# Optimization experiments

Hardware: AMD Instinct MI355X
Metric: run time of the kernel (lower is better)

## Reference

```python
import jax, jax.numpy as jnp
import numpy as np

SOFTMAX_TEMP = 0.01  # config['networks']['matcher_block']['softmax_temp']
B, WINDOW, C, N, WIDTH = 2, 2, 64, 400, 256


def setup_inputs() -> dict:
    key = jax.random.key(0)
    k1, k2, k3 = jax.random.split(key, 3)
    BW = B * WINDOW
    keypoint_scores = jax.random.uniform(k1, (BW, 1, N), dtype=jnp.float32)
    keypoint_desc = jax.random.normal(k2, (BW, C, N), dtype=jnp.float32)
    desc_dense = jax.random.normal(k3, (BW, C, WIDTH, WIDTH), dtype=jnp.float32)
    # pairing indices exactly as built in SoftmaxRefMatcher.__init__
    tgt_ids, src_ids = [], []
    for b in range(B):
        for w in range(WINDOW - 1):
            for t in range(w + 1, WINDOW):
                src_ids.append(w + b * WINDOW)
                tgt_ids.append(t + b * WINDOW)
    return {
        "keypoint_scores": keypoint_scores,
        "keypoint_desc": keypoint_desc,
        "desc_dense": desc_dense,
        "tgt_ids": jnp.array(tgt_ids, dtype=jnp.int32),
        "src_ids": jnp.array(src_ids, dtype=jnp.int32),
    }


def _l2_normalize(x):
    # F.normalize(x, dim=1), eps=1e-12
    return x / jnp.maximum(jnp.linalg.norm(x, axis=1, keepdims=True), 1e-12)


def reference(keypoint_scores, keypoint_desc, desc_dense, tgt_ids, src_ids):
    BW, Cdim, H, W = desc_dense.shape
    HW = H * W
    # src_coords_dense: meshgrid('ij') -> coords[k] = (u=k%W, v=k//W)
    hw = jnp.arange(HW)
    coords = jnp.stack([(hw % W).astype(jnp.float32),
                        (hw // W).astype(jnp.float32)], axis=1)  # [HW, 2]

    src_desc = _l2_normalize(desc_dense.reshape(BW, Cdim, HW))[src_ids]  # [P, C, HW]
    tgt_desc = _l2_normalize(keypoint_desc)[tgt_ids]                     # [P, C, N]

    match_vals = jnp.einsum('pcn,pcm->pnm', tgt_desc, src_desc)          # [P, N, HW]
    soft_match = jax.nn.softmax(match_vals / SOFTMAX_TEMP, axis=2)
    pseudo_coords = jnp.einsum('pnm,mk->pnk', soft_match, coords)        # [P, N, 2]

    tgt_scores = keypoint_scores[tgt_ids]
    return pseudo_coords, tgt_scores, tgt_ids, src_ids
```

## Files before the change

kernel.cpp:

```cpp
#include <hip/hip_runtime.h>
#include <math.h>

#define NPAIR  2
#define KDIM   64
#define NKP    400
#define NPADR  448
#define DSTR   14
#define HWPIX  65536
#define MREF   70.0f
#define LOG2E  1.44269504f

#define AFRAG_DW (NPAIR*DSTR*2*2*2*256)

using frag_ab = __attribute__((ext_vector_type(8))) short;
using f32x4   = __attribute__((ext_vector_type(4))) float;

__device__ __forceinline__ unsigned short f2bf(float f){
    unsigned u = __builtin_bit_cast(unsigned, f);
    u += 0x7fffu + ((u >> 16) & 1u);
    return (unsigned short)(u >> 16);
}
__device__ __forceinline__ float bf2f(unsigned short h){
    unsigned u = ((unsigned)h) << 16;
    return __builtin_bit_cast(float, u);
}
__device__ __forceinline__ float red16(float v){
    v += __builtin_bit_cast(float, __builtin_amdgcn_update_dpp(0, __builtin_bit_cast(int, v), 0xB1,  0xF, 0xF, true));
    v += __builtin_bit_cast(float, __builtin_amdgcn_update_dpp(0, __builtin_bit_cast(int, v), 0x4E,  0xF, 0xF, true));
    v += __builtin_bit_cast(float, __builtin_amdgcn_update_dpp(0, __builtin_bit_cast(int, v), 0x141, 0xF, 0xF, true));
    v += __builtin_bit_cast(float, __builtin_amdgcn_update_dpp(0, __builtin_bit_cast(int, v), 0x140, 0xF, 0xF, true));
    return v;
}

__global__ __launch_bounds__(256) void prep_kernel(
    const float* __restrict__ ksc, const float* __restrict__ kd,
    const int* __restrict__ tgt_ids, const int* __restrict__ src_ids,
    unsigned* __restrict__ wsu, float* __restrict__ out)
{
    __shared__ float xs[KDIM][33];
    __shared__ float inv_s[32];
    int d = blockIdx.x, p = blockIdx.y, t = threadIdx.x;
    int tgt = tgt_ids[p];
    int nl = t & 31, c0 = t >> 5;
    #pragma unroll
    for (int cc = 0; cc < 8; ++cc){
        int c = cc*8 + c0;
        int n = d*32 + nl;
        xs[c][nl] = (n < NKP) ? kd[(tgt*KDIM + c)*NKP + n] : 0.f;
    }
    __syncthreads();
    if (t < 32){
        float s = 0.f;
        #pragma unroll
        for (int c = 0; c < KDIM; ++c){ float v = xs[c][t]; s = fmaf(v, v, s); }
        inv_s[t] = 1.f / fmaxf(sqrtf(s), 1e-12f);
    }
    __syncthreads();
    {
        int l = t & 63, rk = t >> 6;
        int rt = rk >> 1, ks = rk & 1;
        int cl = l & 15, g = l >> 4;
        int nloc = rt*16 + cl;
        float inv = inv_s[nloc];
        int k0 = ks*32 + g*8;
        unsigned hu[4], lu[4];
        #pragma unroll
        for (int j2 = 0; j2 < 4; ++j2){
            float xa = xs[k0 + 2*j2    ][nloc] * inv;
            float xb = xs[k0 + 2*j2 + 1][nloc] * inv;
            unsigned short ha = f2bf(xa), hb = f2bf(xb);
            unsigned short la = f2bf(xa - bf2f(ha)), lb = f2bf(xb - bf2f(hb));
            hu[j2] = (unsigned)ha | ((unsigned)hb << 16);
            lu[j2] = (unsigned)la | ((unsigned)lb << 16);
        }
        unsigned base = (unsigned)((((p*DSTR + d)*2 + rt)*2 + ks)*2)*256 + l*4;
        *(uint4*)&wsu[base]       = make_uint4(hu[0], hu[1], hu[2], hu[3]);
        *(uint4*)&wsu[base + 256] = make_uint4(lu[0], lu[1], lu[2], lu[3]);
    }
    if (t < 32){
        int n = d*32 + t;
        if (n < NKP) out[NPAIR*NKP*2 + p*NKP + n] = ksc[tgt*NKP + n];
    }
    if (d == 0 && t == 0){
        out[NPAIR*NKP*3 + p]         = (float)tgt;
        out[NPAIR*NKP*3 + NPAIR + p] = (float)src_ids[p];
    }
}

__global__ __launch_bounds__(256, 4) void match_kernel(
    const float* __restrict__ dd, const int* __restrict__ src_ids,
    const unsigned* __restrict__ wsu, float* __restrict__ part)
{
    __shared__ unsigned lds[8192];
    __shared__ float ssp[256];
    __shared__ float invn_s[128];
    int mb = blockIdx.x, p = blockIdx.y, t = threadIdx.x;
    const float* plane = dd + (size_t)src_ids[p]*KDIM*HWPIX + mb*128;

    {
        int m = t & 127, kh = t >> 7;
        unsigned sw7 = (unsigned)(m & 7) << 2;
        float ssum = 0.f;
        #pragma unroll
        for (int s2l = 0; s2l < 4; ++s2l){
            int s2 = kh*4 + s2l;
            float v[8];
            #pragma unroll
            for (int j = 0; j < 8; ++j) v[j] = plane[(size_t)(s2*8 + j)*HWPIX + m];
            unsigned hq[4], lq[4];
            #pragma unroll
            for (int q = 0; q < 4; ++q){
                float a = v[2*q], b = v[2*q + 1];
                ssum = fmaf(a, a, ssum);
                ssum = fmaf(b, b, ssum);
                unsigned short ha = f2bf(a), hb = f2bf(b);
                unsigned short la = f2bf(a - bf2f(ha)), lb = f2bf(b - bf2f(hb));
                hq[q] = (unsigned)ha | ((unsigned)hb << 16);
                lq[q] = (unsigned)la | ((unsigned)lb << 16);
            }
            unsigned dwb = (unsigned)m*32 + (((unsigned)s2 << 2) ^ sw7);
            *(uint4*)&lds[dwb]        = make_uint4(hq[0], hq[1], hq[2], hq[3]);
            *(uint4*)&lds[4096 + dwb] = make_uint4(lq[0], lq[1], lq[2], lq[3]);
        }
        ssp[t] = ssum;
    }
    __syncthreads();
    if (t < 128)
        invn_s[t] = (100.f * LOG2E) / fmaxf(sqrtf(ssp[t] + ssp[t + 128]), 1e-12f);
    __syncthreads();

    int w = t >> 6, l = t & 63;
    int cl = l & 15, g = l >> 4;
    int mq = w & 1;
    int mtb = mq << 2;
    const float mref2 = MREF * LOG2E;
    float invm[4];
    #pragma unroll
    for (int mi = 0; mi < 4; ++mi) invm[mi] = invn_s[(mtb + mi)*16 + cl];

    #pragma unroll 1
    for (int d = (w >> 1); d < DSTR; d += 2){
        uint4 AH[2][2], AL[2][2];
        #pragma unroll
        for (int rt = 0; rt < 2; ++rt)
        #pragma unroll
        for (int ks = 0; ks < 2; ++ks){
            unsigned base = (unsigned)((((p*DSTR + d)*2 + rt)*2 + ks)*2)*256 + l*4;
            AH[rt][ks] = *(const uint4*)&wsu[base];
            AL[rt][ks] = *(const uint4*)&wsu[base + 256];
        }
        f32x4 acc[2][4];
        #pragma unroll
        for (int rt = 0; rt < 2; ++rt)
            #pragma unroll
            for (int mi = 0; mi < 4; ++mi)
                acc[rt][mi] = (f32x4){0.f, 0.f, 0.f, 0.f};

        #pragma unroll
        for (int ks = 0; ks < 2; ++ks){
            frag_ab aH0 = __builtin_bit_cast(frag_ab, AH[0][ks]);
            frag_ab aL0 = __builtin_bit_cast(frag_ab, AL[0][ks]);
            frag_ab aH1 = __builtin_bit_cast(frag_ab, AH[1][ks]);
            frag_ab aL1 = __builtin_bit_cast(frag_ab, AL[1][ks]);
            #pragma unroll
            for (int mi = 0; mi < 4; ++mi){
                int mrow = (mtb + mi)*16 + cl;
                unsigned swm = (unsigned)(mrow & 7) << 2;
                unsigned dwb = (unsigned)mrow*32 + (((unsigned)(ks*4 + g) << 2) ^ swm);
                frag_ab BH = __builtin_bit_cast(frag_ab, *(const uint4*)&lds[dwb]);
                frag_ab BL = __builtin_bit_cast(frag_ab, *(const uint4*)&lds[4096 + dwb]);
                acc[0][mi] = __builtin_amdgcn_mfma_f32_16x16x32_bf16(aH0, BH, acc[0][mi], 0, 0, 0);
                acc[1][mi] = __builtin_amdgcn_mfma_f32_16x16x32_bf16(aH1, BH, acc[1][mi], 0, 0, 0);
                acc[0][mi] = __builtin_amdgcn_mfma_f32_16x16x32_bf16(aH0, BL, acc[0][mi], 0, 0, 0);
                acc[1][mi] = __builtin_amdgcn_mfma_f32_16x16x32_bf16(aH1, BL, acc[1][mi], 0, 0, 0);
                acc[0][mi] = __builtin_amdgcn_mfma_f32_16x16x32_bf16(aL0, BH, acc[0][mi], 0, 0, 0);
                acc[1][mi] = __builtin_amdgcn_mfma_f32_16x16x32_bf16(aL1, BH, acc[1][mi], 0, 0, 0);
            }
        }
        #pragma unroll
        for (int rt = 0; rt < 2; ++rt)
        #pragma unroll
        for (int r = 0; r < 4; ++r){
            float sE = 0.f, sU = 0.f;
            #pragma unroll
            for (int mi = 0; mi < 4; ++mi){
                float e = exp2f(fmaf(acc[rt][mi][r], invm[mi], -mref2));
                sE += e;
                sU = fmaf(e, (float)(mi*16), sU);
            }
            sU = fmaf((float)cl, sE, sU);
            sE = red16(sE); sU = red16(sU);
            if (cl == 0){
                int n = d*32 + rt*16 + g*4 + r;
                *(float2*)&part[(((size_t)(p*NPADR + n)*512 + mb)*2 + mq)*2] =
                    make_float2(sE, sU);
            }
        }
    }
}

__global__ __launch_bounds__(256) void merge_kernel(
    const float* __restrict__ part, float* __restrict__ out)
{
    int wid = blockIdx.x*4 + (threadIdx.x >> 6);
    int l = threadIdx.x & 63;
    int p = wid / NKP, n = wid - p*NKP;
    const float* base = part + (size_t)(p*NPADR + n)*2048;
    float S = 0.f, U = 0.f, V = 0.f;
    #pragma unroll
    for (int k = 0; k < 8; ++k){
        int mbk = l + 64*k;
        float4 q = *(const float4*)&base[mbk*4];
        float u0 = (float)((mbk & 1)*128);
        float s = q.x + q.z;
        S += s;
        U += q.y + q.w + u0*q.x + (u0 + 64.f)*q.z;
        V = fmaf((float)(mbk >> 1), s, V);
    }
    #pragma unroll
    for (int off = 1; off < 64; off <<= 1){
        S += __shfl_xor(S, off);
        U += __shfl_xor(U, off);
        V += __shfl_xor(V, off);
    }
    if (l == 0){
        out[(p*NKP + n)*2 + 0] = U / S;
        out[(p*NKP + n)*2 + 1] = V / S;
    }
}

extern "C" void kernel_launch(void* const* d_in, const int* in_sizes, int n_in,
                              void* d_out, int out_size, void* d_ws, size_t ws_size,
                              hipStream_t stream)
{
    const float* ksc     = (const float*)d_in[0];
    const float* kd      = (const float*)d_in[1];
    const float* dd      = (const float*)d_in[2];
    const int*   tgt_ids = (const int*)d_in[3];
    const int*   src_ids = (const int*)d_in[4];
    float* out = (float*)d_out;
    unsigned* wsu = (unsigned*)d_ws;
    float* part = (float*)d_ws + AFRAG_DW;

    prep_kernel <<<dim3(DSTR, NPAIR), 256, 0, stream>>>(ksc, kd, tgt_ids, src_ids, wsu, out);
    match_kernel<<<dim3(512,  NPAIR), 256, 0, stream>>>(dd, src_ids, wsu, part);
    merge_kernel<<<200,               256, 0, stream>>>(part, out);
}
```

Before: 138.3 us.

## Software-pipeline match kernel: hoist B fragments, prefetch A, overlap MFMA with epilogue

```diff
diff --git a/kernel.cpp b/kernel.cpp
--- a/kernel.cpp
+++ b/kernel.cpp
@@ -87,7 +87,7 @@
     }
 }
 
-__global__ __launch_bounds__(256, 4) void match_kernel(
+__global__ __launch_bounds__(256, 3) void match_kernel(
     const float* __restrict__ dd, const int* __restrict__ src_ids,
     const unsigned* __restrict__ wsu, float* __restrict__ part)
 {
@@ -95,6 +95,19 @@
     __shared__ float ssp[256];
     __shared__ float invn_s[128];
     int mb = blockIdx.x, p = blockIdx.y, t = threadIdx.x;
+    int w = t >> 6, l = t & 63;
+    int cl = l & 15, g = l >> 4;
+    int mq = w & 1;
+    int rt = (w >> 1) & 1;
+    int mtb = mq << 2;
+
+    const unsigned* wA = wsu + (size_t)p*28672 + rt*1024 + (unsigned)l*4;
+    uint4 Ae[4], Ao[4];
+    #pragma unroll
+    for (int k = 0; k < 4; ++k) Ae[k] = *(const uint4*)(wA + 0*2048 + k*256);
+    #pragma unroll
+    for (int k = 0; k < 4; ++k) Ao[k] = *(const uint4*)(wA + 1*2048 + k*256);
+
     const float* plane = dd + (size_t)src_ids[p]*KDIM*HWPIX + mb*128;
 
     {
@@ -129,74 +142,80 @@
         invn_s[t] = (100.f * LOG2E) / fmaxf(sqrtf(ssp[t] + ssp[t + 128]), 1e-12f);
     __syncthreads();
 
-    int w = t >> 6, l = t & 63;
-    int cl = l & 15, g = l >> 4;
-    int mq = w & 1;
-    int mtb = mq << 2;
     const float mref2 = MREF * LOG2E;
     float invm[4];
     #pragma unroll
     for (int mi = 0; mi < 4; ++mi) invm[mi] = invn_s[(mtb + mi)*16 + cl];
 
-    #pragma unroll 1
-    for (int d = (w >> 1); d < DSTR; d += 2){
-        uint4 AH[2][2], AL[2][2];
-        #pragma unroll
-        for (int rt = 0; rt < 2; ++rt)
+    uint4 Bf[2][4][2];
+    #pragma unroll
+    for (int ks = 0; ks < 2; ++ks)
+    #pragma unroll
+    for (int mi = 0; mi < 4; ++mi){
+        int mrow = (mtb + mi)*16 + cl;
+        unsigned swm = (unsigned)(mrow & 7) << 2;
+        unsigned dwb = (unsigned)mrow*32 + (((unsigned)(ks*4 + g) << 2) ^ swm);
+        Bf[ks][mi][0] = *(const uint4*)&lds[dwb];
+        Bf[ks][mi][1] = *(const uint4*)&lds[4096 + dwb];
+    }
+
+    f32x4 acc0[4], acc1[4];
+    float* pbase = part + (((size_t)(p*NPADR + rt*16 + g*4)*512 + mb)*2 + mq)*2;
+
+    auto zacc = [&](f32x4* a){
+        #pragma unroll
+        for (int mi = 0; mi < 4; ++mi) a[mi] = (f32x4){0.f,0.f,0.f,0.f};
+    };
+    auto unit = [&](const uint4* A, f32x4* a){
         #pragma unroll
         for (int ks = 0; ks < 2; ++ks){
-            unsigned base = (unsigned)((((p*DSTR + d)*2 + rt)*2 + ks)*2)*256 + l*4;
-            AH[rt][ks] = *(const uint4*)&wsu[base];
-            AL[rt][ks] = *(const uint4*)&wsu[base + 256];
-        }
-        f32x4 acc[2][4];
-        #pragma unroll
-        for (int rt = 0; rt < 2; ++rt)
-            #pragma unroll
-            for (int mi = 0; mi < 4; ++mi)
-                acc[rt][mi] = (f32x4){0.f, 0.f, 0.f, 0.f};
-
-        #pragma unroll
-        for (int ks = 0; ks < 2; ++ks){
-            frag_ab aH0 = __builtin_bit_cast(frag_ab, AH[0][ks]);
-            frag_ab aL0 = __builtin_bit_cast(frag_ab, AL[0][ks]);
-            frag_ab aH1 = __builtin_bit_cast(frag_ab, AH[1][ks]);
-            frag_ab aL1 = __builtin_bit_cast(frag_ab, AL[1][ks]);
+            frag_ab aH = __builtin_bit_cast(frag_ab, A[2*ks]);
+            frag_ab aL = __builtin_bit_cast(frag_ab, A[2*ks + 1]);
             #pragma unroll
             for (int mi = 0; mi < 4; ++mi){
-                int mrow = (mtb + mi)*16 + cl;
-                unsigned swm = (unsigned)(mrow & 7) << 2;
-                unsigned dwb = (unsigned)mrow*32 + (((unsigned)(ks*4 + g) << 2) ^ swm);
-                frag_ab BH = __builtin_bit_cast(frag_ab, *(const uint4*)&lds[dwb]);
-                frag_ab BL = __builtin_bit_cast(frag_ab, *(const uint4*)&lds[4096 + dwb]);
-                acc[0][mi] = __builtin_amdgcn_mfma_f32_16x16x32_bf16(aH0, BH, acc[0][mi], 0, 0, 0);
-                acc[1][mi] = __builtin_amdgcn_mfma_f32_16x16x32_bf16(aH1, BH, acc[1][mi], 0, 0, 0);
-                acc[0][mi] = __builtin_amdgcn_mfma_f32_16x16x32_bf16(aH0, BL, acc[0][mi], 0, 0, 0);
-                acc[1][mi] = __builtin_amdgcn_mfma_f32_16x16x32_bf16(aH1, BL, acc[1][mi], 0, 0, 0);
-                acc[0][mi] = __builtin_amdgcn_mfma_f32_16x16x32_bf16(aL0, BH, acc[0][mi], 0, 0, 0);
-                acc[1][mi] = __builtin_amdgcn_mfma_f32_16x16x32_bf16(aL1, BH, acc[1][mi], 0, 0, 0);
+                frag_ab BH = __builtin_bit_cast(frag_ab, Bf[ks][mi][0]);
+                frag_ab BL = __builtin_bit_cast(frag_ab, Bf[ks][mi][1]);
+                a[mi] = __builtin_amdgcn_mfma_f32_16x16x32_bf16(aH, BH, a[mi], 0, 0, 0);
+                a[mi] = __builtin_amdgcn_mfma_f32_16x16x32_bf16(aH, BL, a[mi], 0, 0, 0);
+                a[mi] = __builtin_amdgcn_mfma_f32_16x16x32_bf16(aL, BH, a[mi], 0, 0, 0);
             }
         }
-        #pragma unroll
-        for (int rt = 0; rt < 2; ++rt)
+    };
+    auto loadA = [&](int d, uint4* A){
+        const unsigned* q = wA + (unsigned)d*2048;
+        #pragma unroll
+        for (int k = 0; k < 4; ++k) A[k] = *(const uint4*)(q + k*256);
+    };
+    auto epi = [&](const f32x4* a, int d){
         #pragma unroll
         for (int r = 0; r < 4; ++r){
             float sE = 0.f, sU = 0.f;
             #pragma unroll
             for (int mi = 0; mi < 4; ++mi){
-                float e = exp2f(fmaf(acc[rt][mi][r], invm[mi], -mref2));
+                float e = exp2f(fmaf(a[mi][r], invm[mi], -mref2));
                 sE += e;
                 sU = fmaf(e, (float)(mi*16), sU);
             }
             sU = fmaf((float)cl, sE, sU);
             sE = red16(sE); sU = red16(sU);
-            if (cl == 0){
-                int n = d*32 + rt*16 + g*4 + r;
-                *(float2*)&part[(((size_t)(p*NPADR + n)*512 + mb)*2 + mq)*2] =
-                    make_float2(sE, sU);
-            }
-        }
-    }
+            if (cl == 0)
+                *(float2*)&pbase[(size_t)(d*32 + r)*2048] = make_float2(sE, sU);
+        }
+    };
+
+    zacc(acc0); unit(Ae, acc0);
+    #pragma unroll 1
+    for (int j = 0; j < 6; ++j){
+        loadA(2*j + 2, Ae);
+        zacc(acc1); unit(Ao, acc1);
+        epi(acc0, 2*j);
+        loadA(2*j + 3, Ao);
+        zacc(acc0); unit(Ae, acc0);
+        epi(acc1, 2*j + 1);
+    }
+    zacc(acc1); unit(Ao, acc1);
+    epi(acc0, 12);
+    epi(acc1, 13);
 }
 
 __global__ __launch_bounds__(256) void merge_kernel(
```

Measured after the change: 135.1 us. 1.02x faster.

## Hold dense-pixel fragments in registers and stream keypoint tiles with double buffering

Applied to the files above, without the earlier changes.

```diff
diff --git a/kernel.cpp b/kernel.cpp
--- a/kernel.cpp
+++ b/kernel.cpp
@@ -4,13 +4,12 @@
 #define NPAIR  2
 #define KDIM   64
 #define NKP    400
-#define NPADR  448
-#define DSTR   14
+#define NTILE  28
 #define HWPIX  65536
 #define MREF   70.0f
 #define LOG2E  1.44269504f
 
-#define AFRAG_DW (NPAIR*DSTR*2*2*2*256)
+#define BFRAG_DW (NPAIR*NTILE*2*2*256)
 
 using frag_ab = __attribute__((ext_vector_type(8))) short;
 using f32x4   = __attribute__((ext_vector_type(4))) float;
@@ -23,13 +22,6 @@
 __device__ __forceinline__ float bf2f(unsigned short h){
     unsigned u = ((unsigned)h) << 16;
     return __builtin_bit_cast(float, u);
-}
-__device__ __forceinline__ float red16(float v){
-    v += __builtin_bit_cast(float, __builtin_amdgcn_update_dpp(0, __builtin_bit_cast(int, v), 0xB1,  0xF, 0xF, true));
-    v += __builtin_bit_cast(float, __builtin_amdgcn_update_dpp(0, __builtin_bit_cast(int, v), 0x4E,  0xF, 0xF, true));
-    v += __builtin_bit_cast(float, __builtin_amdgcn_update_dpp(0, __builtin_bit_cast(int, v), 0x141, 0xF, 0xF, true));
-    v += __builtin_bit_cast(float, __builtin_amdgcn_update_dpp(0, __builtin_bit_cast(int, v), 0x140, 0xF, 0xF, true));
-    return v;
 }
 
 __global__ __launch_bounds__(256) void prep_kernel(
@@ -73,7 +65,8 @@
             hu[j2] = (unsigned)ha | ((unsigned)hb << 16);
             lu[j2] = (unsigned)la | ((unsigned)lb << 16);
         }
-        unsigned base = (unsigned)((((p*DSTR + d)*2 + rt)*2 + ks)*2)*256 + l*4;
+        int nt = d*2 + rt;
+        unsigned base = (unsigned)(((p*NTILE + nt)*2 + ks)*2)*256 + l*4;
         *(uint4*)&wsu[base]       = make_uint4(hu[0], hu[1], hu[2], hu[3]);
         *(uint4*)&wsu[base + 256] = make_uint4(lu[0], lu[1], lu[2], lu[3]);
     }
@@ -95,30 +88,44 @@
     __shared__ float ssp[256];
     __shared__ float invn_s[128];
     int mb = blockIdx.x, p = blockIdx.y, t = threadIdx.x;
+    int w = t >> 6, l = t & 63;
+    int g = l >> 4;
+
+    const unsigned* wB = wsu + (unsigned)p*28672 + (unsigned)l*4;
+    uint4 Bb0[4], Bb1[4];
+    #pragma unroll
+    for (int k = 0; k < 4; ++k) Bb0[k] = *(const uint4*)(wB + k*256);
+    #pragma unroll
+    for (int k = 0; k < 4; ++k) Bb1[k] = *(const uint4*)(wB + 1024 + k*256);
+
     const float* plane = dd + (size_t)src_ids[p]*KDIM*HWPIX + mb*128;
 
     {
         int m = t & 127, kh = t >> 7;
-        unsigned sw7 = (unsigned)(m & 7) << 2;
+        unsigned sw = (unsigned)(m & 7);
         float ssum = 0.f;
+        const float* cp = plane + m + (size_t)kh*32*HWPIX;
         #pragma unroll
         for (int s2l = 0; s2l < 4; ++s2l){
-            int s2 = kh*4 + s2l;
             float v[8];
             #pragma unroll
-            for (int j = 0; j < 8; ++j) v[j] = plane[(size_t)(s2*8 + j)*HWPIX + m];
+            for (int j = 0; j < 8; ++j) v[j] = cp[(size_t)(s2l*8 + j)*HWPIX];
             unsigned hq[4], lq[4];
             #pragma unroll
             for (int q = 0; q < 4; ++q){
-                float a = v[2*q], b = v[2*q + 1];
+                float a = v[2*q], b = v[2*q+1];
                 ssum = fmaf(a, a, ssum);
                 ssum = fmaf(b, b, ssum);
-                unsigned short ha = f2bf(a), hb = f2bf(b);
-                unsigned short la = f2bf(a - bf2f(ha)), lb = f2bf(b - bf2f(hb));
-                hq[q] = (unsigned)ha | ((unsigned)hb << 16);
-                lq[q] = (unsigned)la | ((unsigned)lb << 16);
+                unsigned ta = (__builtin_bit_cast(unsigned, a) + 0x8000u) & 0xFFFF0000u;
+                unsigned tb = (__builtin_bit_cast(unsigned, b) + 0x8000u) & 0xFFFF0000u;
+                float la = a - __builtin_bit_cast(float, ta);
+                float lb = b - __builtin_bit_cast(float, tb);
+                hq[q] = __builtin_amdgcn_perm(tb, ta, 0x07060302u);
+                lq[q] = __builtin_amdgcn_perm(__builtin_bit_cast(unsigned, lb),
+                                              __builtin_bit_cast(unsigned, la), 0x07060302u);
             }
-            unsigned dwb = (unsigned)m*32 + (((unsigned)s2 << 2) ^ sw7);
+            unsigned slot = ((unsigned)(kh*4 + s2l)) ^ sw;
+            unsigned dwb = (unsigned)m*32 + slot*4;
             *(uint4*)&lds[dwb]        = make_uint4(hq[0], hq[1], hq[2], hq[3]);
             *(uint4*)&lds[4096 + dwb] = make_uint4(lq[0], lq[1], lq[2], lq[3]);
         }
@@ -129,103 +136,136 @@
         invn_s[t] = (100.f * LOG2E) / fmaxf(sqrtf(ssp[t] + ssp[t + 128]), 1e-12f);
     __syncthreads();
 
-    int w = t >> 6, l = t & 63;
-    int cl = l & 15, g = l >> 4;
-    int mq = w & 1;
-    int mtb = mq << 2;
+    int mloc0 = w*32;
+    uint4 Ac[2][4];
+    #pragma unroll
+    for (int mt = 0; mt < 2; ++mt){
+        unsigned m = (unsigned)(mloc0 + mt*16 + (l & 15));
+        unsigned sw = m & 7;
+        #pragma unroll
+        for (int k = 0; k < 4; ++k){
+            unsigned slot = (((unsigned)(k >> 1))*4 + (unsigned)g) ^ sw;
+            Ac[mt][k] = *(const uint4*)&lds[(unsigned)(k & 1)*4096 + m*32 + slot*4];
+        }
+    }
+    __syncthreads();
+
     const float mref2 = MREF * LOG2E;
-    float invm[4];
-    #pragma unroll
-    for (int mi = 0; mi < 4; ++mi) invm[mi] = invn_s[(mtb + mi)*16 + cl];
-
+    float invm8[2][4], ub_[2];
+    #pragma unroll
+    for (int mt = 0; mt < 2; ++mt){
+        ub_[mt] = (float)(mloc0 + mt*16 + g*4);
+        #pragma unroll
+        for (int r = 0; r < 4; ++r)
+            invm8[mt][r] = invn_s[mloc0 + mt*16 + g*4 + r];
+    }
+
+    f32x4 acc0[2], acc1[2];
+    float* wp = (float*)lds;
+
+    auto zacc = [&](f32x4* a){
+        a[0] = (f32x4){0.f,0.f,0.f,0.f};
+        a[1] = (f32x4){0.f,0.f,0.f,0.f};
+    };
+    auto unit = [&](const uint4* Bq, f32x4* a2){
+        #pragma unroll
+        for (int ks = 0; ks < 2; ++ks){
+            frag_ab bH  = __builtin_bit_cast(frag_ab, Bq[ks*2]);
+            frag_ab bL  = __builtin_bit_cast(frag_ab, Bq[ks*2 + 1]);
+            frag_ab a0H = __builtin_bit_cast(frag_ab, Ac[0][ks*2]);
+            frag_ab a0L = __builtin_bit_cast(frag_ab, Ac[0][ks*2 + 1]);
+            frag_ab a1H = __builtin_bit_cast(frag_ab, Ac[1][ks*2]);
+            frag_ab a1L = __builtin_bit_cast(frag_ab, Ac[1][ks*2 + 1]);
+            a2[0] = __builtin_amdgcn_mfma_f32_16x16x32_bf16(a0H, bH, a2[0], 0, 0, 0);
+            a2[1] = __builtin_amdgcn_mfma_f32_16x16x32_bf16(a1H, bH, a2[1], 0, 0, 0);
+            a2[0] = __builtin_amdgcn_mfma_f32_16x16x32_bf16(a0H, bL, a2[0], 0, 0, 0);
+            a2[1] = __builtin_amdgcn_mfma_f32_16x16x32_bf16(a1H, bL, a2[1], 0, 0, 0);
+            a2[0] = __builtin_amdgcn_mfma_f32_16x16x32_bf16(a0L, bH, a2[0], 0, 0, 0);
+            a2[1] = __builtin_amdgcn_mfma_f32_16x16x32_bf16(a1L, bH, a2[1], 0, 0, 0);
+        }
+    };
+    auto loadB = [&](int nt, uint4* B){
+        const unsigned* q = wB + (unsigned)nt*1024;
+        #pragma unroll
+        for (int k = 0; k < 4; ++k) B[k] = *(const uint4*)(q + k*256);
+    };
+    auto epi = [&](const f32x4* a2, int nt){
+        float Ssum = 0.f, Usum = 0.f;
+        #pragma unroll
+        for (int mt = 0; mt < 2; ++mt){
+            float e0 = __builtin_amdgcn_exp2f(fmaf(a2[mt][0], invm8[mt][0], -mref2));
+            float e1 = __builtin_amdgcn_exp2f(fmaf(a2[mt][1], invm8[mt][1], -mref2));
+            float e2 = __builtin_amdgcn_exp2f(fmaf(a2[mt][2], invm8[mt][2], -mref2));
+            float e3 = __builtin_amdgcn_exp2f(fmaf(a2[mt][3], invm8[mt][3], -mref2));
+            float Sm = (e0 + e1) + (e2 + e3);
+            float Um = fmaf(e2, 2.f, e1);
+            Um = fmaf(e3, 3.f, Um);
+            Um = fmaf(ub_[mt], Sm, Um);
+            Ssum += Sm; Usum += Um;
+        }
+        Ssum += __shfl_xor(Ssum, 16); Usum += __shfl_xor(Usum, 16);
+        Ssum += __shfl_xor(Ssum, 32); Usum += __shfl_xor(Usum, 32);
+        if (l < 16)
+            *(float2*)&wp[((unsigned)(w*NTILE + nt)*16 + (unsigned)l)*2] =
+                make_float2(Ssum, Usum);
+    };
+
+    zacc(acc0); unit(Bb0, acc0);
     #pragma unroll 1
-    for (int d = (w >> 1); d < DSTR; d += 2){
-        uint4 AH[2][2], AL[2][2];
-        #pragma unroll
-        for (int rt = 0; rt < 2; ++rt)
-        #pragma unroll
-        for (int ks = 0; ks < 2; ++ks){
-            unsigned base = (unsigned)((((p*DSTR + d)*2 + rt)*2 + ks)*2)*256 + l*4;
-            AH[rt][ks] = *(const uint4*)&wsu[base];
-            AL[rt][ks] = *(const uint4*)&wsu[base + 256];
-        }
-        f32x4 acc[2][4];
-        #pragma unroll
-        for (int rt = 0; rt < 2; ++rt)
-            #pragma unroll
-            for (int mi = 0; mi < 4; ++mi)
-                acc[rt][mi] = (f32x4){0.f, 0.f, 0.f, 0.f};
-
-        #pragma unroll
-        for (int ks = 0; ks < 2; ++ks){
-            frag_ab aH0 = __builtin_bit_cast(frag_ab, AH[0][ks]);
-            frag_ab aL0 = __builtin_bit_cast(frag_ab, AL[0][ks]);
-            frag_ab aH1 = __builtin_bit_cast(frag_ab, AH[1][ks]);
-            frag_ab aL1 = __builtin_bit_cast(frag_ab, AL[1][ks]);
-            #pragma unroll
-            for (int mi = 0; mi < 4; ++mi){
-                int mrow = (mtb + mi)*16 + cl;
-                unsigned swm = (unsigned)(mrow & 7) << 2;
-                unsigned dwb = (unsigned)mrow*32 + (((unsigned)(ks*4 + g) << 2) ^ swm);
-                frag_ab BH = __builtin_bit_cast(frag_ab, *(const uint4*)&lds[dwb]);
-                frag_ab BL = __builtin_bit_cast(frag_ab, *(const uint4*)&lds[4096 + dwb]);
-                acc[0][mi] = __builtin_amdgcn_mfma_f32_16x16x32_bf16(aH0, BH, acc[0][mi], 0, 0, 0);
-                acc[1][mi] = __builtin_amdgcn_mfma_f32_16x16x32_bf16(aH1, BH, acc[1][mi], 0, 0, 0);
-                acc[0][mi] = __builtin_amdgcn_mfma_f32_16x16x32_bf16(aH0, BL, acc[0][mi], 0, 0, 0);
-                acc[1][mi] = __builtin_amdgcn_mfma_f32_16x16x32_bf16(aH1, BL, acc[1][mi], 0, 0, 0);
-                acc[0][mi] = __builtin_amdgcn_mfma_f32_16x16x32_bf16(aL0, BH, acc[0][mi], 0, 0, 0);
-                acc[1][mi] = __builtin_amdgcn_mfma_f32_16x16x32_bf16(aL1, BH, acc[1][mi], 0, 0, 0);
-            }
-        }
-        #pragma unroll
-        for (int rt = 0; rt < 2; ++rt)
-        #pragma unroll
-        for (int r = 0; r < 4; ++r){
-            float sE = 0.f, sU = 0.f;
-            #pragma unroll
-            for (int mi = 0; mi < 4; ++mi){
-                float e = exp2f(fmaf(acc[rt][mi][r], invm[mi], -mref2));
-                sE += e;
-                sU = fmaf(e, (float)(mi*16), sU);
-            }
-            sU = fmaf((float)cl, sE, sU);
-            sE = red16(sE); sU = red16(sU);
-            if (cl == 0){
-                int n = d*32 + rt*16 + g*4 + r;
-                *(float2*)&part[(((size_t)(p*NPADR + n)*512 + mb)*2 + mq)*2] =
-                    make_float2(sE, sU);
-            }
-        }
+    for (int j = 0; j < 13; ++j){
+        loadB(2*j + 2, Bb0);
+        zacc(acc1); unit(Bb1, acc1);
+        epi(acc0, 2*j);
+        loadB(2*j + 3, Bb1);
+        zacc(acc0); unit(Bb0, acc0);
+        epi(acc1, 2*j + 1);
+    }
+    zacc(acc1); unit(Bb1, acc1);
+    epi(acc0, 26);
+    epi(acc1, 27);
+
+    __syncthreads();
+    for (int idx = t; idx < NTILE*16; idx += 256){
+        int nt = idx >> 4, cl = idx & 15;
+        float S = 0.f, U = 0.f;
+        #pragma unroll
+        for (int ww = 0; ww < 4; ++ww){
+            float2 q = *(const float2*)&wp[((unsigned)(ww*NTILE + nt)*16 + (unsigned)cl)*2];
+            S += q.x; U += q.y;
+        }
+        *(float2*)&part[(((size_t)p*NTILE + nt)*512 + mb)*32 + cl*2] =
+            make_float2(S, U);
     }
 }
 
 __global__ __launch_bounds__(256) void merge_kernel(
     const float* __restrict__ part, float* __restrict__ out)
 {
-    int wid = blockIdx.x*4 + (threadIdx.x >> 6);
-    int l = threadIdx.x & 63;
-    int p = wid / NKP, n = wid - p*NKP;
-    const float* base = part + (size_t)(p*NPADR + n)*2048;
+    __shared__ float red[3][4][16];
+    int nt = blockIdx.x, p = blockIdx.y, t = threadIdx.x;
+    int j = t & 15, mb0 = t >> 4;
+    const float* base = part + ((size_t)(p*NTILE + nt)*512)*32;
     float S = 0.f, U = 0.f, V = 0.f;
-    #pragma unroll
-    for (int k = 0; k < 8; ++k){
-        int mbk = l + 64*k;
-        float4 q = *(const float4*)&base[mbk*4];
-        float u0 = (float)((mbk & 1)*128);
-        float s = q.x + q.z;
-        S += s;
-        U += q.y + q.w + u0*q.x + (u0 + 64.f)*q.z;
-        V = fmaf((float)(mbk >> 1), s, V);
-    }
-    #pragma unroll
-    for (int off = 1; off < 64; off <<= 1){
-        S += __shfl_xor(S, off);
-        U += __shfl_xor(U, off);
-        V += __shfl_xor(V, off);
-    }
-    if (l == 0){
-        out[(p*NKP + n)*2 + 0] = U / S;
-        out[(p*NKP + n)*2 + 1] = V / S;
+    #pragma unroll 4
+    for (int k = 0; k < 32; ++k){
+        int mbk = mb0 + k*16;
+        float2 q = *(const float2*)&base[(mbk*16 + j)*2];
+        S += q.x;
+        U += q.y + (float)((mbk & 1)*128)*q.x;
+        V = fmaf((float)(mbk >> 1), q.x, V);
+    }
+    S += __shfl_xor(S, 16); U += __shfl_xor(U, 16); V += __shfl_xor(V, 16);
+    S += __shfl_xor(S, 32); U += __shfl_xor(U, 32); V += __shfl_xor(V, 32);
+    int w = t >> 6, l = t & 63;
+    if (l < 16){ red[0][w][j] = S; red[1][w][j] = U; red[2][w][j] = V; }
+    __syncthreads();
+    if (t < 16){
+        float Sf = red[0][0][t] + red[0][1][t] + red[0][2][t] + red[0][3][t];
+        float Uf = red[1][0][t] + red[1][1][t] + red[1][2][t] + red[1][3][t];
+        float Vf = red[2][0][t] + red[2][1][t] + red[2][2][t] + red[2][3][t];
+        int n = nt*16 + t;
+        out[(p*NKP + n)*2 + 0] = Uf / Sf;
+        out[(p*NKP + n)*2 + 1] = Vf / Sf;
     }
 }
 
@@ -240,9 +280,9 @@
     const int*   src_ids = (const int*)d_in[4];
     float* out = (float*)d_out;
     unsigned* wsu = (unsigned*)d_ws;
-    float* part = (float*)d_ws + AFRAG_DW;
-
-    prep_kernel <<<dim3(DSTR, NPAIR), 256, 0, stream>>>(ksc, kd, tgt_ids, src_ids, wsu, out);
-    match_kernel<<<dim3(512,  NPAIR), 256, 0, stream>>>(dd, src_ids, wsu, part);
-    merge_kernel<<<200,               256, 0, stream>>>(part, out);
-}
+    float* part = (float*)d_ws + BFRAG_DW;
+
+    prep_kernel <<<dim3(14, NPAIR),  256, 0, stream>>>(ksc, kd, tgt_ids, src_ids, wsu, out);
+    match_kernel<<<dim3(512, NPAIR), 256, 0, stream>>>(dd, src_ids, wsu, part);
+    merge_kernel<<<dim3(25, NPAIR),  256, 0, stream>>>(part, out);
+}
```

After: 126.6 us. 1.09x faster.
